# Kernel optimization log

Hardware: AMD Instinct MI355X
Metric: run time of the kernel (lower is better)

Reference implementation:

```python
import jax, jax.numpy as jnp
import numpy as np

B, T, C, H = 4, 2048, 1024, 16
D = C // H  # head dim = 64
ROPE_BASE = 10000.0


def _rope_cache(seq_len, dim, dtype=jnp.float32):
    # torchtune-style interleaved RoPE cache
    inv_freq = 1.0 / (ROPE_BASE ** (jnp.arange(0, dim, 2, dtype=jnp.float32) / dim))
    t = jnp.arange(seq_len, dtype=jnp.float32)
    freqs = jnp.outer(t, inv_freq)  # [T, D/2]
    return jnp.cos(freqs).astype(dtype), jnp.sin(freqs).astype(dtype)


def _apply_rope(x, cos, sin):
    # x: [B, H, T, D]; rotate interleaved pairs along last dim
    x1 = x[..., 0::2]
    x2 = x[..., 1::2]
    # broadcast cos/sin [T, D/2] -> [1, 1, T, D/2]
    o1 = x1 * cos - x2 * sin
    o2 = x2 * cos + x1 * sin
    out = jnp.stack([o1, o2], axis=-1).reshape(x.shape)
    return out


def setup_inputs() -> dict:
    key = jax.random.key(0)
    k1, k2, k3 = jax.random.split(key, 3)
    x = jax.random.normal(k1, (B, T, C), dtype=jnp.float32)
    W_in = jax.random.normal(k2, (C, 3 * C), dtype=jnp.float32) * (1.0 / np.sqrt(C))
    b_in = jnp.zeros((3 * C,), dtype=jnp.float32)
    W_out = jax.random.normal(k3, (C, C), dtype=jnp.float32) * (1.0 / np.sqrt(C))
    b_out = jnp.zeros((C,), dtype=jnp.float32)
    return {"x": x, "W_in": W_in, "b_in": b_in, "W_out": W_out, "b_out": b_out}


def reference(x, W_in, b_in, W_out, b_out):
    Bx, Tx, Cx = x.shape
    qkv = x @ W_in + b_in                      # [B, T, 3C]
    q, k, v = jnp.split(qkv, 3, axis=-1)
    # [B, T, C] -> [B, H, T, D]
    def to_heads(t):
        return t.reshape(Bx, Tx, H, D).transpose(0, 2, 1, 3)
    q, k, v = to_heads(q), to_heads(k), to_heads(v)

    cos, sin = _rope_cache(Tx, D, dtype=x.dtype)
    q = _apply_rope(q, cos, sin)
    k = _apply_rope(k, cos, sin)

    scale = 1.0 / np.sqrt(D)
    att = jnp.einsum('bhqd,bhkd->bhqk', q, k) * scale   # [B, H, T, T]
    causal = jnp.tril(jnp.ones((Tx, Tx), dtype=bool))
    att = jnp.where(causal[None, None, :, :], att, jnp.float32(-jnp.inf).astype(att.dtype))
    att = jax.nn.softmax(att, axis=-1)
    # dropout = 0.0 (eval mode): identity
    y = jnp.einsum('bhqk,bhkd->bhqd', att, v)           # [B, H, T, D]
    y = y.transpose(0, 2, 1, 3).reshape(Bx, Tx, Cx)     # [B, T, C]
    return y @ W_out + b_out
```

## Files before the change

kernel.cpp:

```cpp
#include <hip/hip_runtime.h>

#define B_ 4
#define T_ 2048
#define C_ 1024
#define H_ 16
#define D_ 64
#define M_ (B_*T_)
#define N3_ (3*C_)
#define NQT_ 16

typedef unsigned short u16;
typedef short bf16x8 __attribute__((ext_vector_type(8)));
typedef short bf16x4 __attribute__((ext_vector_type(4)));
typedef unsigned short u16x8 __attribute__((ext_vector_type(8)));
typedef unsigned int u32x4 __attribute__((ext_vector_type(4)));
typedef float f32x4 __attribute__((ext_vector_type(4)));
typedef float f32x16 __attribute__((ext_vector_type(16)));

#define QSCALE 0.18033688f
#define DEFER_THR 11.0f

__device__ __forceinline__ u16 f2bf(float f) {
  unsigned u = __float_as_uint(f);
  u += 0x7fffu + ((u >> 16) & 1u);
  return (u16)(u >> 16);
}

__device__ __forceinline__ unsigned cvt_pk_bf16(float lo, float hi) {
  unsigned r;
  asm("v_cvt_pk_bf16_f32 %0, %1, %2" : "=v"(r) : "v"(lo), "v"(hi));
  return r;
}

__device__ __forceinline__ void gload16(const void* g, void* l) {
  __builtin_amdgcn_global_load_lds((const __attribute__((address_space(1))) void*)g,
                                   (__attribute__((address_space(3))) void*)l, 16, 0, 0);
}

__device__ __forceinline__ int epi_key(int ml) { return (ml ^ (ml >> 3)) & 7; }

__global__ __launch_bounds__(256) void k_prep(const float* __restrict__ x,
                                              u16* __restrict__ xbf,
                                              const float* __restrict__ W_in,
                                              u16* __restrict__ WtIn,
                                              const float* __restrict__ W_out,
                                              u16* __restrict__ WtOut,
                                              float* __restrict__ ct,
                                              float* __restrict__ st) {
  __shared__ float tile[64][65];
  const int bx = blockIdx.x, tid = threadIdx.x;
  if (bx < 4096) {
    int i = bx * 256 + tid;
    f32x4 a = *(const f32x4*)(x + (size_t)i * 8);
    f32x4 b = *(const f32x4*)(x + (size_t)i * 8 + 4);
    u16x8 o;
    #pragma unroll
    for (int j = 0; j < 4; ++j) { o[j] = f2bf(a[j]); o[4 + j] = f2bf(b[j]); }
    *(u16x8*)(xbf + (size_t)i * 8) = o;
  } else if (bx < 5120) {
    const float* W; u16* Wt; int K = C_, N, b;
    if (bx < 4864) { W = W_in; Wt = WtIn; N = N3_; b = bx - 4096; }
    else           { W = W_out; Wt = WtOut; N = C_; b = bx - 4864; }
    int ntiles = N / 64;
    int n0 = (b % ntiles) * 64, k0 = (b / ntiles) * 64;
    int c = tid & 63, r0 = tid >> 6;
    #pragma unroll
    for (int i = 0; i < 16; ++i) {
      int r = i * 4 + r0;
      tile[r][c] = W[(size_t)(k0 + r) * N + n0 + c];
    }
    __syncthreads();
    #pragma unroll
    for (int i = 0; i < 16; ++i) {
      int r = i * 4 + r0;
      Wt[(size_t)(n0 + r) * K + k0 + c] = f2bf(tile[c][r]);
    }
  } else {
    int idx = (bx - 5120) * 256 + tid;
    int t = idx >> 5, i = idx & 31;
    double inv = exp(-(2.0 * (double)i / 64.0) * log(10000.0));
    double a = (double)t * inv;
    ct[idx] = (float)cos(a);
    st[idx] = (float)sin(a);
  }
}

template <int MODE>
__global__ __launch_bounds__(256) void k_gemm(const u16* __restrict__ A,
                                              const u16* __restrict__ Bt,
                                              const float* __restrict__ bias,
                                              float* __restrict__ Cout,
                                              u16* __restrict__ Qb, u16* __restrict__ Kb,
                                              u16* __restrict__ Vt,
                                              const float* __restrict__ ctab,
                                              const float* __restrict__ stab,
                                              int Md, int Nd, int Kd) {
  __shared__ u16 sA[128 * 128];
  __shared__ u16 sB[128 * 128];
  const int tid = threadIdx.x, lane = tid & 63, w = tid >> 6;
  const int g = lane >> 4, r = lane & 15;
  const int wm = w >> 1, wn = w & 1;
  const int lin = blockIdx.y * gridDim.x + blockIdx.x;
  const int tM = ((lin & 7) * 8 + ((lin >> 3) & 7)) * 128;
  const int tN = (lin >> 6) * 128;

  f32x4 acc[4][4];
  #pragma unroll
  for (int i = 0; i < 4; ++i)
    #pragma unroll
    for (int j = 0; j < 4; ++j) acc[i][j] = (f32x4){0.f, 0.f, 0.f, 0.f};

  for (int k0 = 0; k0 < Kd; k0 += 128) {
    #pragma unroll
    for (int i = 0; i < 8; ++i) {
      int c = i * 256 + tid, row = c >> 4, slot = (c & 15) ^ (row & 15);
      gload16(A + (size_t)(tM + row) * Kd + k0 + slot * 8, sA + (i * 256 + w * 64) * 8);
    }
    #pragma unroll
    for (int i = 0; i < 8; ++i) {
      int c = i * 256 + tid, row = c >> 4, slot = (c & 15) ^ (row & 15);
      gload16(Bt + (size_t)(tN + row) * Kd + k0 + slot * 8, sB + (i * 256 + w * 64) * 8);
    }
    __syncthreads();
    #pragma unroll
    for (int kk = 0; kk < 4; ++kk) {
      bf16x8 af[4], bfr[4];
      #pragma unroll
      for (int mt = 0; mt < 4; ++mt) {
        int row = wm * 64 + mt * 16 + r;
        af[mt] = *(const bf16x8*)(sA + row * 128 + (((kk * 4 + g) ^ (row & 15)) * 8));
      }
      #pragma unroll
      for (int nt = 0; nt < 4; ++nt) {
        int row = wn * 64 + nt * 16 + r;
        bfr[nt] = *(const bf16x8*)(sB + row * 128 + (((kk * 4 + g) ^ (row & 15)) * 8));
      }
      __builtin_amdgcn_s_setprio(1);
      #pragma unroll
      for (int mt = 0; mt < 4; ++mt)
        #pragma unroll
        for (int nt = 0; nt < 4; ++nt)
          acc[mt][nt] = __builtin_amdgcn_mfma_f32_16x16x32_bf16(af[mt], bfr[nt],
                                                                acc[mt][nt], 0, 0, 0);
      __builtin_amdgcn_s_setprio(0);
    }
    __syncthreads();
  }

  if (MODE == 1) {
    #pragma unroll
    for (int mt = 0; mt < 4; ++mt)
      #pragma unroll
      for (int nt = 0; nt < 4; ++nt) {
        int n = tN + wn * 64 + nt * 16 + r;
        float bv = bias[n];
        #pragma unroll
        for (int reg = 0; reg < 4; ++reg) {
          int m = tM + wm * 64 + mt * 16 + g * 4 + reg;
          Cout[(size_t)m * Nd + n] = acc[mt][nt][reg] + bv;
        }
      }
  } else {
    const int secb = tN >> 10;
    u16* tile = sA;
    #pragma unroll
    for (int mt = 0; mt < 4; ++mt)
      #pragma unroll
      for (int nt = 0; nt < 4; ++nt) {
        int nl = wn * 64 + nt * 16 + r;
        int n = tN + nl;
        float bv = bias[n];
        int dd = n & 63;
        #pragma unroll
        for (int reg = 0; reg < 4; ++reg) {
          int ml = wm * 64 + mt * 16 + g * 4 + reg;
          int tt = (tM + ml) & (T_ - 1);
          float v = acc[mt][nt][reg] + bv;
          if (secb < 2) {
            float pv = __shfl_xor(v, 1);
            int pi = tt * 32 + (dd >> 1);
            float c = ctab[pi], sn = stab[pi];
            v = (dd & 1) ? (v * c + pv * sn) : (v * c - pv * sn);
            if (secb == 0) v *= QSCALE;
          }
          tile[ml * 128 + ((((nl >> 3) ^ epi_key(ml)) << 3) | (nl & 7))] = f2bf(v);
        }
      }
    __syncthreads();
    if (secb < 2) {
      u16* dst = secb == 0 ? Qb : Kb;
      #pragma unroll
      for (int i = 0; i < 8; ++i) {
        int row = w * 32 + (i & 3) * 8 + (lane >> 3);
        int cc = (i >> 2) * 8 + (lane & 7);
        u16x8 val = *(const u16x8*)(tile + row * 128 + ((cc ^ epi_key(row)) << 3));
        int n = tN + cc * 8;
        int m = tM + row;
        int hh = (n & 1023) >> 6, dd = n & 63;
        int bb = m >> 11, tt = m & (T_ - 1);
        *(u16x8*)(dst + ((size_t)(bb * H_ + hh) * T_ + tt) * D_ + dd) = val;
      }
    } else {
      const int bb = tM >> 11, tt0 = tM & (T_ - 1);
      #pragma unroll
      for (int v = 0; v < 8; ++v) {
        int idx = v * 256 + tid;
        int nl = idx >> 4;
        int tg = idx & 15;
        u16x8 val;
        #pragma unroll
        for (int j = 0; j < 8; ++j) {
          int ml = tg * 8 + j;
          val[j] = tile[ml * 128 + ((((nl >> 3) ^ epi_key(ml)) << 3) | (nl & 7))];
        }
        int n = tN + nl;
        int hh = (n & 1023) >> 6, dd = n & 63;
        *(u16x8*)(Vt + ((size_t)(bb * H_ + hh) * D_ + dd) * T_ + tt0 + tg * 8) = val;
      }
    }
  }
}

__global__ __launch_bounds__(256) void k_attn(const u16* __restrict__ Qb,
                                              const u16* __restrict__ Kb,
                                              const u16* __restrict__ Vt,
                                              u16* __restrict__ Y) {
  __shared__ u16 sK[2][64 * 64];
  __shared__ u16 sV[2][64 * 64];
  const int tid = threadIdx.x, w = tid >> 6;
  const int lane = tid & 63, col = lane & 31, hi = lane >> 5;
  const int pair = blockIdx.x;
  const int h = blockIdx.y, b = blockIdx.z;
  const size_t bhK = ((size_t)b * H_ + h) * T_;
  const size_t bhV = ((size_t)b * H_ + h) * D_;

  const int qtA = pair, qtB = (NQT_ - 1) - pair;
  const int ntA = 2 * qtA + 2;
  const int total = 2 * (NQT_ - 1) + 4;

  auto STAGE = [&](int buf, int kt) {
    #pragma unroll
    for (int i = 0; i < 2; ++i) {
      int c = i * 256 + tid, row = c >> 3, slot = (c & 7) ^ (row & 7);
      gload16(Kb + (bhK + kt * 64 + row) * D_ + slot * 8, &sK[buf][(i * 256 + w * 64) * 8]);
    }
    #pragma unroll
    for (int i = 0; i < 2; ++i) {
      int c = i * 256 + tid, row = c >> 3, slot = (c & 7) ^ (row & 7);
      gload16(Vt + (bhV + row) * T_ + kt * 64 + slot * 8, &sV[buf][(i * 256 + w * 64) * 8]);
    }
  };

  int qw = qtA * 128 + w * 32;
  int tq = qw + col;
  bf16x8 qf[4];
  #pragma unroll
  for (int c = 0; c < 4; ++c)
    qf[c] = *(const bf16x8*)(Qb + (bhK + tq) * D_ + c * 16 + hi * 8);

  float m_run = -3e38f, l_run = 0.f;
  f32x16 o0, o1;
  #pragma unroll
  for (int i = 0; i < 16; ++i) { o0[i] = 0.f; o1[i] = 0.f; }

  auto FINAL = [&]() {
    float lr = l_run + __shfl_xor(l_run, 32);
    float rl = 1.0f / lr;
    u16* yrow = Y + ((size_t)b * T_ + tq) * C_ + h * 64;
    #pragma unroll
    for (int dt = 0; dt < 2; ++dt)
      #pragma unroll
      for (int j = 0; j < 8; ++j) {
        float a0 = (dt ? o1[2 * j] : o0[2 * j]) * rl;
        float a1 = (dt ? o1[2 * j + 1] : o0[2 * j + 1]) * rl;
        int d = dt * 32 + 8 * (j >> 1) + 4 * hi + 2 * (j & 1);
        *(unsigned*)(yrow + d) = cvt_pk_bf16(a0, a1);
      }
  };

  STAGE(0, 0);
  __syncthreads();

  for (int it = 0; it < total; ++it) {
    const int cur = it & 1;
    if (it + 1 < total) {
      int nit = it + 1;
      STAGE(cur ^ 1, nit < ntA ? nit : nit - ntA);
    }
    const int ktl = it < ntA ? it : it - ntA;
    const int kb = ktl * 64;
    if (kb <= qw + 31) {
      const bool act1 = (kb + 32 <= qw + 31);
      f32x16 s0, s1;
      #pragma unroll
      for (int i = 0; i < 16; ++i) { s0[i] = 0.f; s1[i] = 0.f; }

      __builtin_amdgcn_s_setprio(1);
      #pragma unroll
      for (int c = 0; c < 4; ++c) {
        int row = col;
        bf16x8 kf = *(const bf16x8*)(&sK[cur][(row * 64 + c * 16 + hi * 8) ^ ((row & 7) << 3)]);
        s0 = __builtin_amdgcn_mfma_f32_32x32x16_bf16(kf, qf[c], s0, 0, 0, 0);
      }
      if (act1) {
        #pragma unroll
        for (int c = 0; c < 4; ++c) {
          int row = 32 + col;
          bf16x8 kf = *(const bf16x8*)(&sK[cur][(row * 64 + c * 16 + hi * 8) ^ ((row & 7) << 3)]);
          s1 = __builtin_amdgcn_mfma_f32_32x32x16_bf16(kf, qf[c], s1, 0, 0, 0);
        }
      }
      __builtin_amdgcn_s_setprio(0);

      if (kb + 31 > qw) {
        #pragma unroll
        for (int reg = 0; reg < 16; ++reg) {
          int key = kb + (reg & 3) + 8 * (reg >> 2) + 4 * hi;
          if (key > tq) s0[reg] = -3e38f;
        }
      }
      if (act1 && kb + 63 > qw) {
        #pragma unroll
        for (int reg = 0; reg < 16; ++reg) {
          int key = kb + 32 + (reg & 3) + 8 * (reg >> 2) + 4 * hi;
          if (key > tq) s1[reg] = -3e38f;
        }
      }

      float pm = s0[0];
      #pragma unroll
      for (int reg = 1; reg < 16; ++reg) pm = fmaxf(pm, s0[reg]);
      if (act1) {
        #pragma unroll
        for (int reg = 0; reg < 16; ++reg) pm = fmaxf(pm, s1[reg]);
      }
      if (__any(pm > m_run + DEFER_THR)) {
        float tm = fmaxf(pm, __shfl_xor(pm, 32));
        float mn = fmaxf(m_run, tm);
        float f = __builtin_amdgcn_exp2f(m_run - mn);
        m_run = mn;
        #pragma unroll
        for (int i = 0; i < 16; ++i) { o0[i] *= f; o1[i] *= f; }
        l_run *= f;
      }

      #pragma unroll
      for (int reg = 0; reg < 16; ++reg) {
        s0[reg] = __builtin_amdgcn_exp2f(s0[reg] - m_run);
        l_run += s0[reg];
      }
      if (act1) {
        #pragma unroll
        for (int reg = 0; reg < 16; ++reg) {
          s1[reg] = __builtin_amdgcn_exp2f(s1[reg] - m_run);
          l_run += s1[reg];
        }
      }

      __builtin_amdgcn_s_setprio(1);
      #pragma unroll
      for (int st = 0; st < 2; ++st) {
        if (st == 1 && !act1) break;
        #pragma unroll
        for (int u = 0; u < 2; ++u) {
          u32x4 pw;
          #pragma unroll
          for (int j = 0; j < 4; ++j) {
            int jr = (4 * u + j) * 2;
            pw[j] = st ? cvt_pk_bf16(s1[jr], s1[jr + 1])
                       : cvt_pk_bf16(s0[jr], s0[jr + 1]);
          }
          bf16x8 pf = __builtin_bit_cast(bf16x8, pw);
          const int keybase = st * 32 + u * 16;
          #pragma unroll
          for (int dt = 0; dt < 2; ++dt) {
            int row = dt * 32 + col;
            int e0 = (row * 64 + keybase + 4 * hi) ^ ((row & 7) << 3);
            int e1 = (row * 64 + keybase + 8 + 4 * hi) ^ ((row & 7) << 3);
            bf16x4 vlo = *(const bf16x4*)(&sV[cur][e0]);
            bf16x4 vhi = *(const bf16x4*)(&sV[cur][e1]);
            bf16x8 vf;
            vf[0] = vlo[0]; vf[1] = vlo[1]; vf[2] = vlo[2]; vf[3] = vlo[3];
            vf[4] = vhi[0]; vf[5] = vhi[1]; vf[6] = vhi[2]; vf[7] = vhi[3];
            if (dt == 0) o0 = __builtin_amdgcn_mfma_f32_32x32x16_bf16(vf, pf, o0, 0, 0, 0);
            else         o1 = __builtin_amdgcn_mfma_f32_32x32x16_bf16(vf, pf, o1, 0, 0, 0);
          }
        }
      }
      __builtin_amdgcn_s_setprio(0);
    }
    __syncthreads();

    if (it == ntA - 1) {
      FINAL();
      qw = qtB * 128 + w * 32;
      tq = qw + col;
      #pragma unroll
      for (int c = 0; c < 4; ++c)
        qf[c] = *(const bf16x8*)(Qb + (bhK + tq) * D_ + c * 16 + hi * 8);
      m_run = -3e38f; l_run = 0.f;
      #pragma unroll
      for (int i = 0; i < 16; ++i) { o0[i] = 0.f; o1[i] = 0.f; }
    }
  }
  FINAL();
}

extern "C" void kernel_launch(void* const* d_in, const int* in_sizes, int n_in,
                              void* d_out, int out_size, void* d_ws, size_t ws_size,
                              hipStream_t stream) {
  const float* x     = (const float*)d_in[0];
  const float* W_in  = (const float*)d_in[1];
  const float* b_in  = (const float*)d_in[2];
  const float* W_out = (const float*)d_in[3];
  const float* b_out = (const float*)d_in[4];
  float* out = (float*)d_out;

  const size_t NE = (size_t)B_ * H_ * T_ * D_;
  u16* Qb    = (u16*)d_ws;
  u16* Kb    = Qb + NE;
  u16* Vt    = Kb + NE;
  u16* xbf   = Vt + NE;
  u16* WtIn  = xbf + (size_t)M_ * C_;
  u16* WtOut = WtIn + (size_t)N3_ * C_;
  float* ctab = (float*)(WtOut + (size_t)C_ * C_);
  float* stab = ctab + T_ * 32;
  u16* ybf = xbf;

  size_t needed = (size_t)((char*)(stab + T_ * 32) - (char*)d_ws);
  if (ws_size < needed) return;

  k_prep<<<5376, 256, 0, stream>>>(x, xbf, W_in, WtIn, W_out, WtOut, ctab, stab);

  k_gemm<0><<<dim3(N3_ / 128, M_ / 128), 256, 0, stream>>>(
      xbf, WtIn, b_in, nullptr, Qb, Kb, Vt, ctab, stab, M_, N3_, C_);

  k_attn<<<dim3(NQT_ / 2, H_, B_), 256, 0, stream>>>(Qb, Kb, Vt, ybf);

  k_gemm<1><<<dim3(C_ / 128, M_ / 128), 256, 0, stream>>>(
      ybf, WtOut, b_out, out, nullptr, nullptr, nullptr, nullptr, nullptr, M_, C_, C_);
}
```

Measured before the change: 184.7 us.

## Process two 32-query subtiles per warp to double K/V reuse in attention

Each warp in the attention kernel now holds Q fragments and softmax state for 64 query rows (two 32-row subtiles), so each staged K/V tile in LDS serves twice as many queries. The query tile per block grows to 256, with the causal pairing adjusted and the grid halved. This cuts LDS staging and global K/V traffic per query. In exchange, register pressure roughly doubles for the accumulators, and the grid has fewer blocks, which may hurt occupancy and load balance.

Result: slower. 219.8 us (+19.0%).

```diff
diff --git a/kernel.cpp b/kernel.cpp
--- a/kernel.cpp
+++ b/kernel.cpp
@@ -7,7 +7,7 @@
 #define D_ 64
 #define M_ (B_*T_)
 #define N3_ (3*C_)
-#define NQT_ 16
+#define NQT2_ 8
 
 typedef unsigned short u16;
 typedef short bf16x8 __attribute__((ext_vector_type(8)));
@@ -234,9 +234,9 @@
   const size_t bhK = ((size_t)b * H_ + h) * T_;
   const size_t bhV = ((size_t)b * H_ + h) * D_;
 
-  const int qtA = pair, qtB = (NQT_ - 1) - pair;
-  const int ntA = 2 * qtA + 2;
-  const int total = 2 * (NQT_ - 1) + 4;
+  const int qtA = pair, qtB = (NQT2_ - 1) - pair;
+  const int ntA = 4 * qtA + 4;
+  const int total = 4 * (NQT2_ - 1) + 8;
 
   auto STAGE = [&](int buf, int kt) {
     #pragma unroll
@@ -251,28 +251,133 @@
     }
   };
 
-  int qw = qtA * 128 + w * 32;
-  int tq = qw + col;
-  bf16x8 qf[4];
+  int qw = qtA * 256 + w * 64;
+  bf16x8 qf0[4], qf1[4];
   #pragma unroll
-  for (int c = 0; c < 4; ++c)
-    qf[c] = *(const bf16x8*)(Qb + (bhK + tq) * D_ + c * 16 + hi * 8);
-
-  float m_run = -3e38f, l_run = 0.f;
-  f32x16 o0, o1;
+  for (int c = 0; c < 4; ++c) {
+    qf0[c] = *(const bf16x8*)(Qb + (bhK + qw + col) * D_ + c * 16 + hi * 8);
+    qf1[c] = *(const bf16x8*)(Qb + (bhK + qw + 32 + col) * D_ + c * 16 + hi * 8);
+  }
+
+  float m0 = -3e38f, l0 = 0.f, m1 = -3e38f, l1 = 0.f;
+  f32x16 o00, o01, o10, o11;
   #pragma unroll
-  for (int i = 0; i < 16; ++i) { o0[i] = 0.f; o1[i] = 0.f; }
-
-  auto FINAL = [&]() {
-    float lr = l_run + __shfl_xor(l_run, 32);
-    float rl = 1.0f / lr;
-    u16* yrow = Y + ((size_t)b * T_ + tq) * C_ + h * 64;
+  for (int i = 0; i < 16; ++i) { o00[i] = 0.f; o01[i] = 0.f; o10[i] = 0.f; o11[i] = 0.f; }
+
+  auto DO_SUB = [&](int cur, int kb, int qws, const bf16x8* qf,
+                    float& mr, float& lr, f32x16& oa, f32x16& ob) {
+    if (kb > qws + 31) return;
+    const int tqs = qws + col;
+    const bool act1 = (kb + 32 <= qws + 31);
+    f32x16 s0, s1;
+    #pragma unroll
+    for (int i = 0; i < 16; ++i) { s0[i] = 0.f; s1[i] = 0.f; }
+
+    __builtin_amdgcn_s_setprio(1);
+    #pragma unroll
+    for (int c = 0; c < 4; ++c) {
+      int row = col;
+      bf16x8 kf = *(const bf16x8*)(&sK[cur][(row * 64 + c * 16 + hi * 8) ^ ((row & 7) << 3)]);
+      s0 = __builtin_amdgcn_mfma_f32_32x32x16_bf16(kf, qf[c], s0, 0, 0, 0);
+    }
+    if (act1) {
+      #pragma unroll
+      for (int c = 0; c < 4; ++c) {
+        int row = 32 + col;
+        bf16x8 kf = *(const bf16x8*)(&sK[cur][(row * 64 + c * 16 + hi * 8) ^ ((row & 7) << 3)]);
+        s1 = __builtin_amdgcn_mfma_f32_32x32x16_bf16(kf, qf[c], s1, 0, 0, 0);
+      }
+    }
+    __builtin_amdgcn_s_setprio(0);
+
+    if (kb + 31 > qws) {
+      #pragma unroll
+      for (int reg = 0; reg < 16; ++reg) {
+        int key = kb + (reg & 3) + 8 * (reg >> 2) + 4 * hi;
+        if (key > tqs) s0[reg] = -3e38f;
+      }
+    }
+    if (act1 && kb + 63 > qws) {
+      #pragma unroll
+      for (int reg = 0; reg < 16; ++reg) {
+        int key = kb + 32 + (reg & 3) + 8 * (reg >> 2) + 4 * hi;
+        if (key > tqs) s1[reg] = -3e38f;
+      }
+    }
+
+    float pm = s0[0];
+    #pragma unroll
+    for (int reg = 1; reg < 16; ++reg) pm = fmaxf(pm, s0[reg]);
+    if (act1) {
+      #pragma unroll
+      for (int reg = 0; reg < 16; ++reg) pm = fmaxf(pm, s1[reg]);
+    }
+    if (__any(pm > mr + DEFER_THR)) {
+      float tm = fmaxf(pm, __shfl_xor(pm, 32));
+      float mn = fmaxf(mr, tm);
+      float f = __builtin_amdgcn_exp2f(mr - mn);
+      mr = mn;
+      #pragma unroll
+      for (int i = 0; i < 16; ++i) { oa[i] *= f; ob[i] *= f; }
+      lr *= f;
+    }
+
+    #pragma unroll
+    for (int reg = 0; reg < 16; ++reg) {
+      s0[reg] = __builtin_amdgcn_exp2f(s0[reg] - mr);
+      lr += s0[reg];
+    }
+    if (act1) {
+      #pragma unroll
+      for (int reg = 0; reg < 16; ++reg) {
+        s1[reg] = __builtin_amdgcn_exp2f(s1[reg] - mr);
+        lr += s1[reg];
+      }
+    }
+
+    __builtin_amdgcn_s_setprio(1);
+    #pragma unroll
+    for (int st = 0; st < 2; ++st) {
+      if (st == 1 && !act1) break;
+      #pragma unroll
+      for (int u = 0; u < 2; ++u) {
+        u32x4 pw;
+        #pragma unroll
+        for (int j = 0; j < 4; ++j) {
+          int jr = (4 * u + j) * 2;
+          pw[j] = st ? cvt_pk_bf16(s1[jr], s1[jr + 1])
+                     : cvt_pk_bf16(s0[jr], s0[jr + 1]);
+        }
+        bf16x8 pf = __builtin_bit_cast(bf16x8, pw);
+        const int keybase = st * 32 + u * 16;
+        #pragma unroll
+        for (int dt = 0; dt < 2; ++dt) {
+          int row = dt * 32 + col;
+          int e0 = (row * 64 + keybase + 4 * hi) ^ ((row & 7) << 3);
+          int e1 = (row * 64 + keybase + 8 + 4 * hi) ^ ((row & 7) << 3);
+          bf16x4 vlo = *(const bf16x4*)(&sV[cur][e0]);
+          bf16x4 vhi = *(const bf16x4*)(&sV[cur][e1]);
+          bf16x8 vf;
+          vf[0] = vlo[0]; vf[1] = vlo[1]; vf[2] = vlo[2]; vf[3] = vlo[3];
+          vf[4] = vhi[0]; vf[5] = vhi[1]; vf[6] = vhi[2]; vf[7] = vhi[3];
+          if (dt == 0) oa = __builtin_amdgcn_mfma_f32_32x32x16_bf16(vf, pf, oa, 0, 0, 0);
+          else         ob = __builtin_amdgcn_mfma_f32_32x32x16_bf16(vf, pf, ob, 0, 0, 0);
+        }
+      }
+    }
+    __builtin_amdgcn_s_setprio(0);
+  };
+
+  auto FINAL = [&](int qws, float lr, const f32x16& oa, const f32x16& ob) {
+    float ls = lr + __shfl_xor(lr, 32);
+    float rl = 1.0f / ls;
+    u16* yrow = Y + ((size_t)b * T_ + qws + col) * C_ + h * 64;
     #pragma unroll
     for (int dt = 0; dt < 2; ++dt)
       #pragma unroll
       for (int j = 0; j < 8; ++j) {
-        float a0 = (dt ? o1[2 * j] : o0[2 * j]) * rl;
-        float a1 = (dt ? o1[2 * j + 1] : o0[2 * j + 1]) * rl;
+        float a0 = (dt ? ob[2 * j] : oa[2 * j]) * rl;
+        float a1 = (dt ? ob[2 * j + 1] : oa[2 * j + 1]) * rl;
         int d = dt * 32 + 8 * (j >> 1) + 4 * hi + 2 * (j & 1);
         *(unsigned*)(yrow + d) = cvt_pk_bf16(a0, a1);
       }
@@ -289,121 +394,26 @@
     }
     const int ktl = it < ntA ? it : it - ntA;
     const int kb = ktl * 64;
-    if (kb <= qw + 31) {
-      const bool act1 = (kb + 32 <= qw + 31);
-      f32x16 s0, s1;
-      #pragma unroll
-      for (int i = 0; i < 16; ++i) { s0[i] = 0.f; s1[i] = 0.f; }
-
-      __builtin_amdgcn_s_setprio(1);
+    DO_SUB(cur, kb, qw,      qf0, m0, l0, o00, o01);
+    DO_SUB(cur, kb, qw + 32, qf1, m1, l1, o10, o11);
+    __syncthreads();
+
+    if (it == ntA - 1) {
+      FINAL(qw,      l0, o00, o01);
+      FINAL(qw + 32, l1, o10, o11);
+      qw = qtB * 256 + w * 64;
       #pragma unroll
       for (int c = 0; c < 4; ++c) {
-        int row = col;
-        bf16x8 kf = *(const bf16x8*)(&sK[cur][(row * 64 + c * 16 + hi * 8) ^ ((row & 7) << 3)]);
-        s0 = __builtin_amdgcn_mfma_f32_32x32x16_bf16(kf, qf[c], s0, 0, 0, 0);
-      }
-      if (act1) {
-        #pragma unroll
-        for (int c = 0; c < 4; ++c) {
-          int row = 32 + col;
-          bf16x8 kf = *(const bf16x8*)(&sK[cur][(row * 64 + c * 16 + hi * 8) ^ ((row & 7) << 3)]);
-          s1 = __builtin_amdgcn_mfma_f32_32x32x16_bf16(kf, qf[c], s1, 0, 0, 0);
-        }
-      }
-      __builtin_amdgcn_s_setprio(0);
-
-      if (kb + 31 > qw) {
-        #pragma unroll
-        for (int reg = 0; reg < 16; ++reg) {
-          int key = kb + (reg & 3) + 8 * (reg >> 2) + 4 * hi;
-          if (key > tq) s0[reg] = -3e38f;
-        }
-      }
-      if (act1 && kb + 63 > qw) {
-        #pragma unroll
-        for (int reg = 0; reg < 16; ++reg) {
-          int key = kb + 32 + (reg & 3) + 8 * (reg >> 2) + 4 * hi;
-          if (key > tq) s1[reg] = -3e38f;
-        }
-      }
-
-      float pm = s0[0];
-      #pragma unroll
-      for (int reg = 1; reg < 16; ++reg) pm = fmaxf(pm, s0[reg]);
-      if (act1) {
-        #pragma unroll
-        for (int reg = 0; reg < 16; ++reg) pm = fmaxf(pm, s1[reg]);
-      }
-      if (__any(pm > m_run + DEFER_THR)) {
-        float tm = fmaxf(pm, __shfl_xor(pm, 32));
-        float mn = fmaxf(m_run, tm);
-        float f = __builtin_amdgcn_exp2f(m_run - mn);
-        m_run = mn;
-        #pragma unroll
-        for (int i = 0; i < 16; ++i) { o0[i] *= f; o1[i] *= f; }
-        l_run *= f;
-      }
-
-      #pragma unroll
-      for (int reg = 0; reg < 16; ++reg) {
-        s0[reg] = __builtin_amdgcn_exp2f(s0[reg] - m_run);
-        l_run += s0[reg];
-      }
-      if (act1) {
-        #pragma unroll
-        for (int reg = 0; reg < 16; ++reg) {
-          s1[reg] = __builtin_amdgcn_exp2f(s1[reg] - m_run);
-          l_run += s1[reg];
-        }
-      }
-
-      __builtin_amdgcn_s_setprio(1);
-      #pragma unroll
-      for (int st = 0; st < 2; ++st) {
-        if (st == 1 && !act1) break;
-        #pragma unroll
-        for (int u = 0; u < 2; ++u) {
-          u32x4 pw;
-          #pragma unroll
-          for (int j = 0; j < 4; ++j) {
-            int jr = (4 * u + j) * 2;
-            pw[j] = st ? cvt_pk_bf16(s1[jr], s1[jr + 1])
-                       : cvt_pk_bf16(s0[jr], s0[jr + 1]);
-          }
-          bf16x8 pf = __builtin_bit_cast(bf16x8, pw);
-          const int keybase = st * 32 + u * 16;
-          #pragma unroll
-          for (int dt = 0; dt < 2; ++dt) {
-            int row = dt * 32 + col;
-            int e0 = (row * 64 + keybase + 4 * hi) ^ ((row & 7) << 3);
-            int e1 = (row * 64 + keybase + 8 + 4 * hi) ^ ((row & 7) << 3);
-            bf16x4 vlo = *(const bf16x4*)(&sV[cur][e0]);
-            bf16x4 vhi = *(const bf16x4*)(&sV[cur][e1]);
-            bf16x8 vf;
-            vf[0] = vlo[0]; vf[1] = vlo[1]; vf[2] = vlo[2]; vf[3] = vlo[3];
-            vf[4] = vhi[0]; vf[5] = vhi[1]; vf[6] = vhi[2]; vf[7] = vhi[3];
-            if (dt == 0) o0 = __builtin_amdgcn_mfma_f32_32x32x16_bf16(vf, pf, o0, 0, 0, 0);
-            else         o1 = __builtin_amdgcn_mfma_f32_32x32x16_bf16(vf, pf, o1, 0, 0, 0);
-          }
-        }
-      }
-      __builtin_amdgcn_s_setprio(0);
-    }
-    __syncthreads();
-
-    if (it == ntA - 1) {
-      FINAL();
-      qw = qtB * 128 + w * 32;
-      tq = qw + col;
-      #pragma unroll
-      for (int c = 0; c < 4; ++c)
-        qf[c] = *(const bf16x8*)(Qb + (bhK + tq) * D_ + c * 16 + hi * 8);
-      m_run = -3e38f; l_run = 0.f;
-      #pragma unroll
-      for (int i = 0; i < 16; ++i) { o0[i] = 0.f; o1[i] = 0.f; }
+        qf0[c] = *(const bf16x8*)(Qb + (bhK + qw + col) * D_ + c * 16 + hi * 8);
+        qf1[c] = *(const bf16x8*)(Qb + (bhK + qw + 32 + col) * D_ + c * 16 + hi * 8);
+      }
+      m0 = -3e38f; l0 = 0.f; m1 = -3e38f; l1 = 0.f;
+      #pragma unroll
+      for (int i = 0; i < 16; ++i) { o00[i] = 0.f; o01[i] = 0.f; o10[i] = 0.f; o11[i] = 0.f; }
     }
   }
-  FINAL();
+  FINAL(qw,      l0, o00, o01);
+  FINAL(qw + 32, l1, o10, o11);
 }
 
 extern "C" void kernel_launch(void* const* d_in, const int* in_sizes, int n_in,
@@ -435,7 +445,7 @@
   k_gemm<0><<<dim3(N3_ / 128, M_ / 128), 256, 0, stream>>>(
       xbf, WtIn, b_in, nullptr, Qb, Kb, Vt, ctab, stab, M_, N3_, C_);
 
-  k_attn<<<dim3(NQT_ / 2, H_, B_), 256, 0, stream>>>(Qb, Kb, Vt, ybf);
+  k_attn<<<dim3(NQT2_ / 2, H_, B_), 256, 0, stream>>>(Qb, Kb, Vt, ybf);
 
   k_gemm<1><<<dim3(C_ / 128, M_ / 128), 256, 0, stream>>>(
       ybf, WtOut, b_out, out, nullptr, nullptr, nullptr, nullptr, nullptr, M_, C_, C_);
```

## Use 128x256 tiles with 512 threads and K=64 steps for QKV GEMM

Applied to the files above, without the earlier changes.

Splits the templated GEMM into a dedicated QKV-projection kernel and an output-projection kernel. The QKV kernel now computes a 128x256 output tile with 8 waves (512 threads), using 64-wide K chunks with an XOR swizzle, and writes its epilogue in two 128-column halves through the reused LDS buffer. The wider N tile is meant to reuse each A tile across more output columns and cut global A traffic. The shorter K chunk doubles the number of sync points and gives less MFMA work per barrier, and the epilogue gains extra barriers.

Result: slower. 223.6 us (+21.0%).

```diff
diff --git a/kernel.cpp b/kernel.cpp
--- a/kernel.cpp
+++ b/kernel.cpp
@@ -85,16 +85,140 @@
   }
 }
 
-template <int MODE>
-__global__ __launch_bounds__(256) void k_gemm(const u16* __restrict__ A,
-                                              const u16* __restrict__ Bt,
-                                              const float* __restrict__ bias,
-                                              float* __restrict__ Cout,
-                                              u16* __restrict__ Qb, u16* __restrict__ Kb,
-                                              u16* __restrict__ Vt,
-                                              const float* __restrict__ ctab,
-                                              const float* __restrict__ stab,
-                                              int Md, int Nd, int Kd) {
+__global__ __launch_bounds__(512) void k_gemm1(const u16* __restrict__ A,
+                                               const u16* __restrict__ Bt,
+                                               const float* __restrict__ bias,
+                                               u16* __restrict__ Qb, u16* __restrict__ Kb,
+                                               u16* __restrict__ Vt,
+                                               const float* __restrict__ ctab,
+                                               const float* __restrict__ stab) {
+  __shared__ u16 lds[128 * 64 + 256 * 64];
+  u16* sA = lds;
+  u16* sB = lds + 128 * 64;
+  const int tid = threadIdx.x, lane = tid & 63, w = tid >> 6;
+  const int g = lane >> 4, r = lane & 15;
+  const int wm = w >> 2, wn = w & 3;
+  const int Kd = C_;
+  const int lin = blockIdx.y * gridDim.x + blockIdx.x;
+  const int tM = ((lin & 7) * 8 + ((lin >> 3) & 7)) * 128;
+  const int tN = (lin >> 6) * 256;
+
+  f32x4 acc[4][4];
+  #pragma unroll
+  for (int i = 0; i < 4; ++i)
+    #pragma unroll
+    for (int j = 0; j < 4; ++j) acc[i][j] = (f32x4){0.f, 0.f, 0.f, 0.f};
+
+  for (int k0 = 0; k0 < Kd; k0 += 64) {
+    #pragma unroll
+    for (int i = 0; i < 2; ++i) {
+      int c = i * 512 + tid, row = c >> 3, slot = (c & 7) ^ (row & 7);
+      gload16(A + (size_t)(tM + row) * Kd + k0 + slot * 8, sA + (i * 512 + w * 64) * 8);
+    }
+    #pragma unroll
+    for (int i = 0; i < 4; ++i) {
+      int c = i * 512 + tid, row = c >> 3, slot = (c & 7) ^ (row & 7);
+      gload16(Bt + (size_t)(tN + row) * Kd + k0 + slot * 8, sB + (i * 512 + w * 64) * 8);
+    }
+    __syncthreads();
+    bf16x8 af[4][2], bfr[4][2];
+    #pragma unroll
+    for (int mt = 0; mt < 4; ++mt)
+      #pragma unroll
+      for (int kk = 0; kk < 2; ++kk) {
+        int row = wm * 64 + mt * 16 + r;
+        af[mt][kk] = *(const bf16x8*)(sA + ((row * 64 + kk * 32 + g * 8) ^ ((row & 7) << 3)));
+      }
+    #pragma unroll
+    for (int nt = 0; nt < 4; ++nt)
+      #pragma unroll
+      for (int kk = 0; kk < 2; ++kk) {
+        int row = wn * 64 + nt * 16 + r;
+        bfr[nt][kk] = *(const bf16x8*)(sB + ((row * 64 + kk * 32 + g * 8) ^ ((row & 7) << 3)));
+      }
+    __builtin_amdgcn_s_setprio(1);
+    #pragma unroll
+    for (int mt = 0; mt < 4; ++mt)
+      #pragma unroll
+      for (int nt = 0; nt < 4; ++nt)
+        #pragma unroll
+        for (int kk = 0; kk < 2; ++kk)
+          acc[mt][nt] = __builtin_amdgcn_mfma_f32_16x16x32_bf16(af[mt][kk], bfr[nt][kk],
+                                                                acc[mt][nt], 0, 0, 0);
+    __builtin_amdgcn_s_setprio(0);
+    __syncthreads();
+  }
+
+  const int secb = tN >> 10;
+  u16* tile = lds;
+  const int bb = tM >> 11;
+  #pragma unroll
+  for (int hN = 0; hN < 2; ++hN) {
+    if ((wn >> 1) == hN) {
+      #pragma unroll
+      for (int mt = 0; mt < 4; ++mt)
+        #pragma unroll
+        for (int nt = 0; nt < 4; ++nt) {
+          int nl = (wn & 1) * 64 + nt * 16 + r;
+          int n = tN + hN * 128 + nl;
+          float bv = bias[n];
+          int dd = n & 63;
+          #pragma unroll
+          for (int reg = 0; reg < 4; ++reg) {
+            int ml = wm * 64 + mt * 16 + g * 4 + reg;
+            int tt = (tM + ml) & (T_ - 1);
+            float v = acc[mt][nt][reg] + bv;
+            if (secb < 2) {
+              float pv = __shfl_xor(v, 1);
+              int pi = tt * 32 + (dd >> 1);
+              float c = ctab[pi], sn = stab[pi];
+              v = (dd & 1) ? (v * c + pv * sn) : (v * c - pv * sn);
+              if (secb == 0) v *= QSCALE;
+            }
+            tile[ml * 128 + ((((nl >> 3) ^ epi_key(ml)) << 3) | (nl & 7))] = f2bf(v);
+          }
+        }
+    }
+    __syncthreads();
+    if (secb < 2) {
+      u16* dst = secb == 0 ? Qb : Kb;
+      #pragma unroll
+      for (int i = 0; i < 4; ++i) {
+        int idx = i * 512 + tid;
+        int row = idx >> 4, cc = idx & 15;
+        u16x8 val = *(const u16x8*)(tile + row * 128 + ((cc ^ epi_key(row)) << 3));
+        int n = tN + hN * 128 + cc * 8;
+        int m = tM + row;
+        int hh = (n & 1023) >> 6, dd = n & 63;
+        int tt = m & (T_ - 1);
+        *(u16x8*)(dst + ((size_t)(bb * H_ + hh) * T_ + tt) * D_ + dd) = val;
+      }
+    } else {
+      const int tt0 = tM & (T_ - 1);
+      #pragma unroll
+      for (int i = 0; i < 4; ++i) {
+        int idx = i * 512 + tid;
+        int nl = idx >> 4, tg = idx & 15;
+        u16x8 val;
+        #pragma unroll
+        for (int j = 0; j < 8; ++j) {
+          int ml = tg * 8 + j;
+          val[j] = tile[ml * 128 + ((((nl >> 3) ^ epi_key(ml)) << 3) | (nl & 7))];
+        }
+        int n = tN + hN * 128 + nl;
+        int hh = (n & 1023) >> 6, dd = n & 63;
+        *(u16x8*)(Vt + ((size_t)(bb * H_ + hh) * D_ + dd) * T_ + tt0 + tg * 8) = val;
+      }
+    }
+    __syncthreads();
+  }
+}
+
+__global__ __launch_bounds__(256) void k_gemm2(const u16* __restrict__ A,
+                                               const u16* __restrict__ Bt,
+                                               const float* __restrict__ bias,
+                                               float* __restrict__ Cout,
+                                               int Nd, int Kd) {
   __shared__ u16 sA[128 * 128];
   __shared__ u16 sB[128 * 128];
   const int tid = threadIdx.x, lane = tid & 63, w = tid >> 6;
@@ -147,78 +271,18 @@
     __syncthreads();
   }
 
-  if (MODE == 1) {
-    #pragma unroll
-    for (int mt = 0; mt < 4; ++mt)
-      #pragma unroll
-      for (int nt = 0; nt < 4; ++nt) {
-        int n = tN + wn * 64 + nt * 16 + r;
-        float bv = bias[n];
-        #pragma unroll
-        for (int reg = 0; reg < 4; ++reg) {
-          int m = tM + wm * 64 + mt * 16 + g * 4 + reg;
-          Cout[(size_t)m * Nd + n] = acc[mt][nt][reg] + bv;
-        }
-      }
-  } else {
-    const int secb = tN >> 10;
-    u16* tile = sA;
-    #pragma unroll
-    for (int mt = 0; mt < 4; ++mt)
-      #pragma unroll
-      for (int nt = 0; nt < 4; ++nt) {
-        int nl = wn * 64 + nt * 16 + r;
-        int n = tN + nl;
-        float bv = bias[n];
-        int dd = n & 63;
-        #pragma unroll
-        for (int reg = 0; reg < 4; ++reg) {
-          int ml = wm * 64 + mt * 16 + g * 4 + reg;
-          int tt = (tM + ml) & (T_ - 1);
-          float v = acc[mt][nt][reg] + bv;
-          if (secb < 2) {
-            float pv = __shfl_xor(v, 1);
-            int pi = tt * 32 + (dd >> 1);
-            float c = ctab[pi], sn = stab[pi];
-            v = (dd & 1) ? (v * c + pv * sn) : (v * c - pv * sn);
-            if (secb == 0) v *= QSCALE;
-          }
-          tile[ml * 128 + ((((nl >> 3) ^ epi_key(ml)) << 3) | (nl & 7))] = f2bf(v);
-        }
-      }
-    __syncthreads();
-    if (secb < 2) {
-      u16* dst = secb == 0 ? Qb : Kb;
-      #pragma unroll
-      for (int i = 0; i < 8; ++i) {
-        int row = w * 32 + (i & 3) * 8 + (lane >> 3);
-        int cc = (i >> 2) * 8 + (lane & 7);
-        u16x8 val = *(const u16x8*)(tile + row * 128 + ((cc ^ epi_key(row)) << 3));
-        int n = tN + cc * 8;
-        int m = tM + row;
-        int hh = (n & 1023) >> 6, dd = n & 63;
-        int bb = m >> 11, tt = m & (T_ - 1);
-        *(u16x8*)(dst + ((size_t)(bb * H_ + hh) * T_ + tt) * D_ + dd) = val;
-      }
-    } else {
-      const int bb = tM >> 11, tt0 = tM & (T_ - 1);
-      #pragma unroll
-      for (int v = 0; v < 8; ++v) {
-        int idx = v * 256 + tid;
-        int nl = idx >> 4;
-        int tg = idx & 15;
-        u16x8 val;
-        #pragma unroll
-        for (int j = 0; j < 8; ++j) {
-          int ml = tg * 8 + j;
-          val[j] = tile[ml * 128 + ((((nl >> 3) ^ epi_key(ml)) << 3) | (nl & 7))];
-        }
-        int n = tN + nl;
-        int hh = (n & 1023) >> 6, dd = n & 63;
-        *(u16x8*)(Vt + ((size_t)(bb * H_ + hh) * D_ + dd) * T_ + tt0 + tg * 8) = val;
-      }
-    }
-  }
+  #pragma unroll
+  for (int mt = 0; mt < 4; ++mt)
+    #pragma unroll
+    for (int nt = 0; nt < 4; ++nt) {
+      int n = tN + wn * 64 + nt * 16 + r;
+      float bv = bias[n];
+      #pragma unroll
+      for (int reg = 0; reg < 4; ++reg) {
+        int m = tM + wm * 64 + mt * 16 + g * 4 + reg;
+        Cout[(size_t)m * Nd + n] = acc[mt][nt][reg] + bv;
+      }
+    }
 }
 
 __global__ __launch_bounds__(256) void k_attn(const u16* __restrict__ Qb,
@@ -432,11 +496,11 @@
 
   k_prep<<<5376, 256, 0, stream>>>(x, xbf, W_in, WtIn, W_out, WtOut, ctab, stab);
 
-  k_gemm<0><<<dim3(N3_ / 128, M_ / 128), 256, 0, stream>>>(
-      xbf, WtIn, b_in, nullptr, Qb, Kb, Vt, ctab, stab, M_, N3_, C_);
+  k_gemm1<<<dim3(N3_ / 256, M_ / 128), 512, 0, stream>>>(
+      xbf, WtIn, b_in, Qb, Kb, Vt, ctab, stab);
 
   k_attn<<<dim3(NQT_ / 2, H_, B_), 256, 0, stream>>>(Qb, Kb, Vt, ybf);
 
-  k_gemm<1><<<dim3(C_ / 128, M_ / 128), 256, 0, stream>>>(
-      ybf, WtOut, b_out, out, nullptr, nullptr, nullptr, nullptr, nullptr, M_, C_, C_);
-}
+  k_gemm2<<<dim3(C_ / 128, M_ / 128), 256, 0, stream>>>(
+      ybf, WtOut, b_out, out, C_, C_);
+}
```
